# Kernel optimization log

Hardware: AMD Instinct MI355X
Metric: run time of the kernel (lower is better)

## Reference

```python
import jax, jax.numpy as jnp
import numpy as np

HID = 200
HALF = 100  # TreeLSTM hidden = hidden_size // 2
N_EDUS = 32768
N_STEPS = 2 * N_EDUS - 1


def setup_inputs() -> dict:
    key = jax.random.key(0)
    ks = jax.random.split(key, 16)
    s = 0.05  # keep logits / gates in a sane range
    d = {}
    d["enc_cls"] = jax.random.normal(ks[0], (N_EDUS, 768), jnp.float32)
    d["W_proj"] = jax.random.normal(ks[1], (HID, 768), jnp.float32) * s
    d["b_proj"] = jax.random.normal(ks[2], (HID,), jnp.float32) * s
    d["missing_node"] = jax.random.uniform(ks[3], (HID,), jnp.float32)
    d["W_act"] = jax.random.normal(ks[4], (2, 3 * HID), jnp.float32) * s
    d["b_act"] = jax.random.normal(ks[5], (2,), jnp.float32) * s
    d["W_lab"] = jax.random.normal(ks[6], (19, 3 * HID), jnp.float32) * s
    d["b_lab"] = jax.random.normal(ks[7], (19,), jnp.float32) * s
    d["W_dir"] = jax.random.normal(ks[8], (3, 3 * HID), jnp.float32) * s
    d["b_dir"] = jax.random.normal(ks[9], (3,), jnp.float32) * s
    d["W_tree"] = jax.random.normal(ks[10], (5 * HALF, 2 * HALF), jnp.float32) * s
    d["b_tree"] = jax.random.normal(ks[11], (5 * HALF,), jnp.float32) * s
    d["gold_action"] = jax.random.randint(ks[12], (N_STEPS,), 0, 2, jnp.int32)
    d["gold_label"] = jax.random.randint(ks[13], (N_STEPS,), 0, 19, jnp.int32)
    d["gold_direction"] = jax.random.randint(ks[14], (N_STEPS,), 0, 3, jnp.int32)
    return d


def reference(enc_cls, W_proj, b_proj, missing_node, W_act, b_act,
              W_lab, b_lab, W_dir, b_dir, W_tree, b_tree,
              gold_action, gold_label, gold_direction):
    N = enc_cls.shape[0]
    S = 2 * N - 1
    # BERT CLS -> project (dropout is identity in eval)
    enc = enc_cls @ W_proj.T + b_proj  # [N, 200]

    # deterministic left-branching gold schedule: shift, then (shift, reduce)*
    t = jnp.arange(S)
    is_shift = (t == 0) | (t % 2 == 1)

    def treelstm(e1, e2):
        # embeddings are concat(h, c), each HALF
        h1, c1 = e1[:HALF], e1[HALF:]
        h2, c2 = e2[:HALF], e2[HALF:]
        g = W_tree @ jnp.concatenate([h1, h2]) + b_tree  # [5*HALF]
        i, f1, f2, o, u = jnp.split(g, 5)
        c = jax.nn.sigmoid(i) * jnp.tanh(u) \
            + jax.nn.sigmoid(f1) * c1 + jax.nn.sigmoid(f2) * c2
        h = jax.nn.sigmoid(o) * jnp.tanh(c)
        return jnp.concatenate([h, c])

    def ce(logits, y):
        # CrossEntropyLoss for a single example
        return jax.nn.logsumexp(logits) - logits[y]

    def step(carry, xs):
        s1, s0, ptr = carry
        shift, ga, gl, gd = xs
        b = jnp.where(ptr < N, enc[jnp.minimum(ptr, N - 1)], missing_node)
        feats = jnp.concatenate([s1, s0, b])  # [600]
        loss = (ce(W_act @ feats + b_act, ga)
                + ce(W_lab @ feats + b_lab, gl)
                + ce(W_dir @ feats + b_dir, gd))
        merged = treelstm(s1, s0)
        s0n = jnp.where(shift, b, merged)
        s1n = jnp.where(shift, s0, missing_node)
        ptrn = ptr + shift.astype(ptr.dtype)
        return (s1n, s0n, ptrn), loss

    init = (missing_node, missing_node, jnp.int32(0))
    (_, root, _), losses = jax.lax.scan(
        step, init, (is_shift, gold_action, gold_label, gold_direction))
    return losses.sum()
```

## Files before the change

kernel.cpp:

```cpp
#include <hip/hip_runtime.h>
#include <cstdint>

#define HID 200
#define HALF 100
#define N_EDUS 32768
#define N_STEPS (2*N_EDUS - 1)
#define KMAX 32766
#define PSTRIDE 500

typedef __fp16 h2v __attribute__((ext_vector_type(2)));
typedef _Float16 f16x8 __attribute__((ext_vector_type(8)));
typedef float f32x4 __attribute__((ext_vector_type(4)));

__global__ __launch_bounds__(256) void gemm_bt(const float* __restrict__ A, int lda,
    const float* __restrict__ B, int ldb, const float* __restrict__ bias,
    float* __restrict__ C, int ldc, int M, int N, int K)
{
    __shared__ float As[32][68];
    __shared__ float Bs[32][68];
    const int tid = threadIdx.x;
    const int tx = tid & 15, ty = tid >> 4;
    const int m0 = blockIdx.x * 64, n0 = blockIdx.y * 64;
    float acc[4][4] = {};
    for (int kc = 0; kc < K; kc += 32) {
        const int kk = tid & 31, r0 = tid >> 5;
        #pragma unroll
        for (int p = 0; p < 8; ++p) {
            const int mm = r0 + p * 8;
            const int m = m0 + mm, n = n0 + mm, kg = kc + kk;
            As[kk][mm] = (m < M && kg < K) ? A[(size_t)m * lda + kg] : 0.f;
            Bs[kk][mm] = (n < N && kg < K) ? B[(size_t)n * ldb + kg] : 0.f;
        }
        __syncthreads();
        #pragma unroll
        for (int kk2 = 0; kk2 < 32; ++kk2) {
            const float4 a = *(const float4*)&As[kk2][tx * 4];
            const float4 b = *(const float4*)&Bs[kk2][ty * 4];
            const float av[4] = {a.x, a.y, a.z, a.w};
            const float bv[4] = {b.x, b.y, b.z, b.w};
            #pragma unroll
            for (int r = 0; r < 4; ++r)
                #pragma unroll
                for (int c = 0; c < 4; ++c)
                    acc[r][c] += av[r] * bv[c];
        }
        __syncthreads();
    }
    #pragma unroll
    for (int r = 0; r < 4; ++r) {
        const int m = m0 + tx * 4 + r;
        if (m >= M) continue;
        #pragma unroll
        for (int c = 0; c < 4; ++c) {
            const int n = n0 + ty * 4 + c;
            if (n < N) C[(size_t)m * ldc + n] = acc[r][c] + (bias ? bias[n] : 0.f);
        }
    }
}

__global__ void prep_kernel(const float* __restrict__ W_act, const float* __restrict__ W_lab,
    const float* __restrict__ W_dir, const float* __restrict__ miss,
    float* __restrict__ WAB, float* __restrict__ WBC,
    float* __restrict__ msAB, float* __restrict__ msBC, float* __restrict__ out)
{
    const int tid = threadIdx.x;
    if (tid == 0) out[0] = 0.f;
    for (int i = tid; i < 48 * 200; i += 256) {
        const int r = i / 200, c = i % 200;
        const int rr = r % 24;
        const float* src = (rr < 2) ? (W_act + rr * 600)
                         : (rr < 21) ? (W_lab + (rr - 2) * 600)
                                     : (W_dir + (rr - 21) * 600);
        WAB[i] = src[c + (r < 24 ? 0 : 200)];
        WBC[i] = src[c + (r < 24 ? 200 : 400)];
    }
    __syncthreads();
    if (tid < 48) {
        float sA = 0.f, sB = 0.f;
        for (int c = 0; c < 200; ++c) {
            sA += WAB[tid * 200 + c] * miss[c];
            sB += WBC[tid * 200 + c] * miss[c];
        }
        msAB[tid] = sA;
        msBC[tid] = sB;
    }
}

__global__ __launch_bounds__(256) void pack_wb(const float* __restrict__ W_tree,
                                               uint4* __restrict__ WB)
{
    const int i = blockIdx.x * 256 + threadIdx.x;
    if (i >= 8960) return;
    const int lane = i & 63, f = i >> 6;
    const int kc = f & 3, gw = f >> 2;
    const int g = gw % 5, w = gw / 5;
    const int row = w * 16 + (lane & 15);
    const int kb = kc * 32 + (lane >> 4) * 8;
    unsigned int dws[4];
    #pragma unroll
    for (int dw = 0; dw < 4; ++dw) {
        const int k0 = kb + dw * 2;
        float w0 = 0.f, w1 = 0.f;
        if (row < 100) {
            const float* Wr = W_tree + (size_t)(g * 100 + row) * 200;
            if (k0 < 100)     w0 = Wr[k0];
            if (k0 + 1 < 100) w1 = Wr[k0 + 1];
        }
        h2v h = __builtin_amdgcn_cvt_pkrtz(w0, w1);
        __builtin_memcpy(&dws[dw], &h, 4);
    }
    uint4 v; v.x = dws[0]; v.y = dws[1]; v.z = dws[2]; v.w = dws[3];
    WB[i] = v;
}

__device__ __forceinline__ float sigf(float x) {
    return __builtin_amdgcn_rcpf(1.f + __expf(-x));
}
__device__ __forceinline__ float tanhf_(float x) {
    return 1.f - 2.f * __builtin_amdgcn_rcpf(1.f + __expf(2.f * x));
}

#define BAR() asm volatile("s_waitcnt lgkmcnt(0)\n\ts_barrier" ::: "memory")

#define BODY(U, DOLOAD) \
{ \
    const uint4* hb = (const uint4*)(&hbuf[(U) & 1][0]); \
    f16x8 bb[4]; \
    { \
        uint4 t0 = hb[kgrp];      uint4 t1 = hb[4 + kgrp]; \
        uint4 t2 = hb[8 + kgrp];  uint4 t3 = hb[12 + kgrp]; \
        __builtin_memcpy(&bb[0], &t0, 16); __builtin_memcpy(&bb[1], &t1, 16); \
        __builtin_memcpy(&bb[2], &t2, 16); __builtin_memcpy(&bb[3], &t3, 16); \
    } \
    f32x4 aA[5], aB[5]; \
    _Pragma("unroll") \
    for (int g = 0; g < 5; ++g) \
        aA[g] = __builtin_amdgcn_mfma_f32_16x16x32_f16(bb[0], Wf[g][0], z4, 0, 0, 0); \
    _Pragma("unroll") \
    for (int g = 0; g < 5; ++g) \
        aB[g] = __builtin_amdgcn_mfma_f32_16x16x32_f16(bb[2], Wf[g][2], z4, 0, 0, 0); \
    _Pragma("unroll") \
    for (int g = 0; g < 5; ++g) \
        aA[g] = __builtin_amdgcn_mfma_f32_16x16x32_f16(bb[1], Wf[g][1], aA[g], 0, 0, 0); \
    _Pragma("unroll") \
    for (int g = 0; g < 5; ++g) \
        aB[g] = __builtin_amdgcn_mfma_f32_16x16x32_f16(bb[3], Wf[g][3], aB[g], 0, 0, 0); \
    const float gi  = aA[0][0] + aB[0][0] + pr[U][0]; \
    const float gf1 = aA[1][0] + aB[1][0] + pr[U][1]; \
    const float gf2 = aA[2][0] + aB[2][0] + pr[U][2]; \
    const float go  = aA[3][0] + aB[3][0] + pr[U][3]; \
    const float gu  = aA[4][0] + aB[4][0] + pr[U][4]; \
    const float c2v = pr[U][5]; \
    if (DOLOAD) { \
        pr[U][0] = pP[0];   pr[U][1] = pP[100]; pr[U][2] = pP[200]; \
        pr[U][3] = pP[300]; pr[U][4] = pP[400]; pP += PSTRIDE; \
        pr[U][5] = *pE; pE += HID; \
    } \
    const float cnew = sigf(gi) * tanhf_(gu) + sigf(gf1) * c_sel + sigf(gf2) * c2v; \
    const float hnew = sigf(go) * tanhf_(cnew); \
    c_sel = cnew; \
    if (act) { \
        pM[0] = hnew; pM[100] = cnew; \
        hbuf[((U) & 1) ^ 1][r] = (_Float16)hnew; \
    } \
    pM += HID; \
    BAR(); \
}

__attribute__((amdgpu_flat_work_group_size(448, 448), amdgpu_waves_per_eu(2, 2)))
__global__ void chain_kernel(const float* __restrict__ enc,
    const uint4* __restrict__ WB, const float* __restrict__ P, float* __restrict__ M)
{
    const int T = threadIdx.x;
    const int wave = T >> 6, lane = T & 63;
    const int col = lane & 15, kgrp = lane >> 4;
    const int r = wave * 16 + col;
    const int rc = (r < 100) ? r : 99;
    const bool act = (kgrp == 0) && (r < 100);
    __shared__ __align__(16) _Float16 hbuf[2][128];

    if (T < 200) M[T] = enc[T];
    if (T < 128) {
        hbuf[0][T] = (T < 100) ? (_Float16)enc[T] : (_Float16)0.f;
        hbuf[1][T] = (_Float16)0.f;
    }

    f16x8 Wf[5][4];
    #pragma unroll
    for (int g = 0; g < 5; ++g)
        #pragma unroll
        for (int kc = 0; kc < 4; ++kc) {
            uint4 tt = WB[(((wave * 5 + g) * 4) + kc) * 64 + lane];
            __builtin_memcpy(&Wf[g][kc], &tt, 16);
        }
    f32x4 z4 = {0.f, 0.f, 0.f, 0.f};

    float c_sel = enc[100 + rc];

    float pr[4][6];
    #pragma unroll
    for (int u = 0; u < 4; ++u) {
        #pragma unroll
        for (int g = 0; g < 5; ++g)
            pr[u][g] = P[(size_t)(1 + u) * PSTRIDE + g * 100 + rc];
        pr[u][5] = enc[(size_t)(1 + u) * HID + 100 + rc];
    }
    const float* pP = P + (size_t)5 * PSTRIDE + rc;
    const float* pE = enc + (size_t)5 * HID + 100 + rc;
    float* pM = M + HID + r;
    BAR();

    for (int base = 1; base <= KMAX - 9; base += 4) {
        BODY(0, true);
        BODY(1, true);
        BODY(2, true);
        BODY(3, true);
    }
    BODY(0, true);
    BODY(1, true);
    BODY(2, false);
    BODY(3, false);
    BODY(0, false);
    BODY(1, false);
}

__global__ __launch_bounds__(256) void loss_kernel(const float* __restrict__ TM,
    const float* __restrict__ TE, const float* __restrict__ msAB, const float* __restrict__ msBC,
    const float* __restrict__ b_act, const float* __restrict__ b_lab, const float* __restrict__ b_dir,
    const int* __restrict__ ga, const int* __restrict__ gl, const int* __restrict__ gd,
    float* __restrict__ out)
{
    const int t = blockIdx.x * 256 + threadIdx.x;
    float loss = 0.f;
    if (t < N_STEPS) {
        const float *v1, *v0, *vb;
        if (t == 0)      { v1 = msAB; v0 = msAB + 24; vb = TE + 24; }
        else if (t == 1) { v1 = msAB; v0 = TE;        vb = TE + 48 + 24; }
        else if ((t & 1) == 0) {
            const int k = t >> 1;
            v1 = TM + (size_t)(k - 1) * 48;
            v0 = TE + (size_t)k * 48;
            vb = (k < N_EDUS - 1) ? (TE + (size_t)(k + 1) * 48 + 24) : (msBC + 24);
        } else {
            const int k = t >> 1;
            v1 = msAB;
            v0 = TM + (size_t)k * 48 + 24;
            vb = TE + (size_t)(k + 1) * 48 + 24;
        }
        float l[24];
        #pragma unroll
        for (int j = 0; j < 24; ++j) l[j] = v1[j] + v0[j] + vb[j];
        l[0] += b_act[0]; l[1] += b_act[1];
        #pragma unroll
        for (int j = 0; j < 19; ++j) l[2 + j] += b_lab[j];
        #pragma unroll
        for (int j = 0; j < 3; ++j) l[21 + j] += b_dir[j];
        const int ya = ga[t], yl = gl[t], yd = gd[t];
        {
            const float m = fmaxf(l[0], l[1]);
            const float sum = __expf(l[0] - m) + __expf(l[1] - m);
            loss += m + __logf(sum) - (ya == 0 ? l[0] : l[1]);
        }
        {
            float m = l[2];
            #pragma unroll
            for (int j = 1; j < 19; ++j) m = fmaxf(m, l[2 + j]);
            float sum = 0.f, ly = 0.f;
            #pragma unroll
            for (int j = 0; j < 19; ++j) {
                sum += __expf(l[2 + j] - m);
                if (j == yl) ly = l[2 + j];
            }
            loss += m + __logf(sum) - ly;
        }
        {
            const float m = fmaxf(fmaxf(l[21], l[22]), l[23]);
            const float sum = __expf(l[21] - m) + __expf(l[22] - m) + __expf(l[23] - m);
            const float ly = (yd == 0) ? l[21] : (yd == 1 ? l[22] : l[23]);
            loss += m + __logf(sum) - ly;
        }
    }
    #pragma unroll
    for (int off = 32; off > 0; off >>= 1) loss += __shfl_down(loss, off, 64);
    __shared__ float wsum[4];
    const int lane = threadIdx.x & 63, wv = threadIdx.x >> 6;
    if (lane == 0) wsum[wv] = loss;
    __syncthreads();
    if (threadIdx.x == 0) atomicAdd(out, wsum[0] + wsum[1] + wsum[2] + wsum[3]);
}

extern "C" void kernel_launch(void* const* d_in, const int* in_sizes, int n_in,
                              void* d_out, int out_size, void* d_ws, size_t ws_size,
                              hipStream_t stream) {
    const float* enc_cls = (const float*)d_in[0];
    const float* W_proj  = (const float*)d_in[1];
    const float* b_proj  = (const float*)d_in[2];
    const float* miss    = (const float*)d_in[3];
    const float* W_act   = (const float*)d_in[4];
    const float* b_act   = (const float*)d_in[5];
    const float* W_lab   = (const float*)d_in[6];
    const float* b_lab   = (const float*)d_in[7];
    const float* W_dir   = (const float*)d_in[8];
    const float* b_dir   = (const float*)d_in[9];
    const float* W_tree  = (const float*)d_in[10];
    const float* b_tree  = (const float*)d_in[11];
    const int*   ga      = (const int*)d_in[12];
    const int*   gl      = (const int*)d_in[13];
    const int*   gd      = (const int*)d_in[14];
    float* out = (float*)d_out;

    float* ws   = (float*)d_ws;
    float* enc  = ws;
    float* Mar  = ws + 6553600;
    float* P    = ws + 13107000;
    float* WAB  = ws + 29490500;
    float* WBC  = WAB + 9600;
    float* msAB = WBC + 9600;
    float* msBC = msAB + 48;
    uint4* WB   = (uint4*)(msBC + 48);
    float* TM = P;
    float* TE = P + 1572816;

    gemm_bt<<<dim3(512, 4, 1), 256, 0, stream>>>(enc_cls, 768, W_proj, 768, b_proj,
                                                 enc, 200, N_EDUS, 200, 768);
    gemm_bt<<<dim3(512, 8, 1), 256, 0, stream>>>(enc + 200, 200, W_tree + 100, 200, b_tree,
                                                 P + PSTRIDE, PSTRIDE, KMAX, 500, 100);
    prep_kernel<<<1, 256, 0, stream>>>(W_act, W_lab, W_dir, miss, WAB, WBC, msAB, msBC, out);
    pack_wb<<<35, 256, 0, stream>>>(W_tree, WB);
    chain_kernel<<<1, 448, 0, stream>>>(enc, WB, P, Mar);
    gemm_bt<<<dim3(512, 1, 1), 256, 0, stream>>>(Mar, 200, WAB, 200, nullptr,
                                                 TM, 48, KMAX + 1, 48, 200);
    gemm_bt<<<dim3(512, 1, 1), 256, 0, stream>>>(enc, 200, WBC, 200, nullptr,
                                                 TE, 48, N_EDUS, 48, 200);
    loss_kernel<<<dim3(256, 1, 1), 256, 0, stream>>>(TM, TE, msAB, msBC,
                                                     b_act, b_lab, b_dir, ga, gl, gd, out);
}
```

Baseline: 19.33 ms.

## Interleave gate and h/c layouts for vector loads and single MFMA chain

The precomputed gate buffer P is written in an interleaved layout (four gates contiguous per row), so the serial chain kernel fetches them with one float4 plus one scalar load instead of five strided loads. The merged-node output M stores h and c interleaved as a float2, and the loss-side weight matrix WAB and its missing-node dot product are permuted to match. The MFMA accumulation becomes a single dependent chain over the four k-chunks instead of two partial chains, and the prefetch of next-step values moves ahead of the MFMAs. The aim is to cut per-step memory instructions on the latency-bound serial loop, at the cost of a longer MFMA dependency chain.

```diff
diff --git a/kernel.cpp b/kernel.cpp
--- a/kernel.cpp
+++ b/kernel.cpp
@@ -14,7 +14,7 @@
 
 __global__ __launch_bounds__(256) void gemm_bt(const float* __restrict__ A, int lda,
     const float* __restrict__ B, int ldb, const float* __restrict__ bias,
-    float* __restrict__ C, int ldc, int M, int N, int K)
+    float* __restrict__ C, int ldc, int M, int N, int K, int scat)
 {
     __shared__ float As[32][68];
     __shared__ float Bs[32][68];
@@ -53,7 +53,15 @@
         #pragma unroll
         for (int c = 0; c < 4; ++c) {
             const int n = n0 + ty * 4 + c;
-            if (n < N) C[(size_t)m * ldc + n] = acc[r][c] + (bias ? bias[n] : 0.f);
+            if (n < N) {
+                const float v = acc[r][c] + (bias ? bias[n] : 0.f);
+                int col = n;
+                if (scat) {
+                    const int q = n / 100, rr = n - q * 100;
+                    col = (q < 4) ? rr * 4 + q : 400 + rr;
+                }
+                C[(size_t)m * ldc + col] = v;
+            }
         }
     }
 }
@@ -71,14 +79,15 @@
         const float* src = (rr < 2) ? (W_act + rr * 600)
                          : (rr < 21) ? (W_lab + (rr - 2) * 600)
                                      : (W_dir + (rr - 21) * 600);
-        WAB[i] = src[c + (r < 24 ? 0 : 200)];
+        const int ci = (c >> 1) + (c & 1) * 100;
+        WAB[i] = src[ci + (r < 24 ? 0 : 200)];
         WBC[i] = src[c + (r < 24 ? 200 : 400)];
     }
     __syncthreads();
     if (tid < 48) {
         float sA = 0.f, sB = 0.f;
         for (int c = 0; c < 200; ++c) {
-            sA += WAB[tid * 200 + c] * miss[c];
+            sA += WAB[tid * 200 + c] * miss[(c >> 1) + (c & 1) * 100];
             sB += WBC[tid * 200 + c] * miss[c];
         }
         msAB[tid] = sA;
@@ -132,35 +141,35 @@
         __builtin_memcpy(&bb[0], &t0, 16); __builtin_memcpy(&bb[1], &t1, 16); \
         __builtin_memcpy(&bb[2], &t2, 16); __builtin_memcpy(&bb[3], &t3, 16); \
     } \
-    f32x4 aA[5], aB[5]; \
+    const float p0 = pr[U][0], p1 = pr[U][1], p2 = pr[U][2]; \
+    const float p3 = pr[U][3], p4 = pr[U][4], c2v = pr[U][5]; \
+    if (DOLOAD) { \
+        const float4 g4 = *(const float4*)pP4; \
+        pr[U][0] = g4.x; pr[U][1] = g4.y; pr[U][2] = g4.z; pr[U][3] = g4.w; \
+        pr[U][4] = *pPu; \
+        pP4 += PSTRIDE; pPu += PSTRIDE; \
+        pr[U][5] = *pE; pE += HID; \
+    } \
+    f32x4 acc[5]; \
     _Pragma("unroll") \
     for (int g = 0; g < 5; ++g) \
-        aA[g] = __builtin_amdgcn_mfma_f32_16x16x32_f16(bb[0], Wf[g][0], z4, 0, 0, 0); \
+        acc[g] = __builtin_amdgcn_mfma_f32_16x16x32_f16(bb[0], Wf[g][0], z4, 0, 0, 0); \
     _Pragma("unroll") \
-    for (int g = 0; g < 5; ++g) \
-        aB[g] = __builtin_amdgcn_mfma_f32_16x16x32_f16(bb[2], Wf[g][2], z4, 0, 0, 0); \
-    _Pragma("unroll") \
-    for (int g = 0; g < 5; ++g) \
-        aA[g] = __builtin_amdgcn_mfma_f32_16x16x32_f16(bb[1], Wf[g][1], aA[g], 0, 0, 0); \
-    _Pragma("unroll") \
-    for (int g = 0; g < 5; ++g) \
-        aB[g] = __builtin_amdgcn_mfma_f32_16x16x32_f16(bb[3], Wf[g][3], aB[g], 0, 0, 0); \
-    const float gi  = aA[0][0] + aB[0][0] + pr[U][0]; \
-    const float gf1 = aA[1][0] + aB[1][0] + pr[U][1]; \
-    const float gf2 = aA[2][0] + aB[2][0] + pr[U][2]; \
-    const float go  = aA[3][0] + aB[3][0] + pr[U][3]; \
-    const float gu  = aA[4][0] + aB[4][0] + pr[U][4]; \
-    const float c2v = pr[U][5]; \
-    if (DOLOAD) { \
-        pr[U][0] = pP[0];   pr[U][1] = pP[100]; pr[U][2] = pP[200]; \
-        pr[U][3] = pP[300]; pr[U][4] = pP[400]; pP += PSTRIDE; \
-        pr[U][5] = *pE; pE += HID; \
-    } \
+    for (int kc = 1; kc < 4; ++kc) \
+        _Pragma("unroll") \
+        for (int g = 0; g < 5; ++g) \
+            acc[g] = __builtin_amdgcn_mfma_f32_16x16x32_f16(bb[kc], Wf[g][kc], acc[g], 0, 0, 0); \
+    const float gi  = acc[0][0] + p0; \
+    const float gf1 = acc[1][0] + p1; \
+    const float gf2 = acc[2][0] + p2; \
+    const float go  = acc[3][0] + p3; \
+    const float gu  = acc[4][0] + p4; \
     const float cnew = sigf(gi) * tanhf_(gu) + sigf(gf1) * c_sel + sigf(gf2) * c2v; \
     const float hnew = sigf(go) * tanhf_(cnew); \
     c_sel = cnew; \
     if (act) { \
-        pM[0] = hnew; pM[100] = cnew; \
+        float2 hc; hc.x = hnew; hc.y = cnew; \
+        *(float2*)pM = hc; \
         hbuf[((U) & 1) ^ 1][r] = (_Float16)hnew; \
     } \
     pM += HID; \
@@ -179,7 +188,10 @@
     const bool act = (kgrp == 0) && (r < 100);
     __shared__ __align__(16) _Float16 hbuf[2][128];
 
-    if (T < 200) M[T] = enc[T];
+    if (T < 100) {
+        float2 hc; hc.x = enc[T]; hc.y = enc[100 + T];
+        *(float2*)(M + 2 * T) = hc;
+    }
     if (T < 128) {
         hbuf[0][T] = (T < 100) ? (_Float16)enc[T] : (_Float16)0.f;
         hbuf[1][T] = (_Float16)0.f;
@@ -200,14 +212,16 @@
     float pr[4][6];
     #pragma unroll
     for (int u = 0; u < 4; ++u) {
-        #pragma unroll
-        for (int g = 0; g < 5; ++g)
-            pr[u][g] = P[(size_t)(1 + u) * PSTRIDE + g * 100 + rc];
+        const float* pu4 = P + (size_t)(1 + u) * PSTRIDE + rc * 4;
+        const float4 g4 = *(const float4*)pu4;
+        pr[u][0] = g4.x; pr[u][1] = g4.y; pr[u][2] = g4.z; pr[u][3] = g4.w;
+        pr[u][4] = P[(size_t)(1 + u) * PSTRIDE + 400 + rc];
         pr[u][5] = enc[(size_t)(1 + u) * HID + 100 + rc];
     }
-    const float* pP = P + (size_t)5 * PSTRIDE + rc;
-    const float* pE = enc + (size_t)5 * HID + 100 + rc;
-    float* pM = M + HID + r;
+    const float* pP4 = P + (size_t)5 * PSTRIDE + rc * 4;
+    const float* pPu = P + (size_t)5 * PSTRIDE + 400 + rc;
+    const float* pE  = enc + (size_t)5 * HID + 100 + rc;
+    float* pM = M + HID + 2 * r;
     BAR();
 
     for (int base = 1; base <= KMAX - 9; base += 4) {
@@ -322,16 +336,16 @@
     float* TE = P + 1572816;
 
     gemm_bt<<<dim3(512, 4, 1), 256, 0, stream>>>(enc_cls, 768, W_proj, 768, b_proj,
-                                                 enc, 200, N_EDUS, 200, 768);
+                                                 enc, 200, N_EDUS, 200, 768, 0);
     gemm_bt<<<dim3(512, 8, 1), 256, 0, stream>>>(enc + 200, 200, W_tree + 100, 200, b_tree,
-                                                 P + PSTRIDE, PSTRIDE, KMAX, 500, 100);
+                                                 P + PSTRIDE, PSTRIDE, KMAX, 500, 100, 1);
     prep_kernel<<<1, 256, 0, stream>>>(W_act, W_lab, W_dir, miss, WAB, WBC, msAB, msBC, out);
     pack_wb<<<35, 256, 0, stream>>>(W_tree, WB);
     chain_kernel<<<1, 448, 0, stream>>>(enc, WB, P, Mar);
     gemm_bt<<<dim3(512, 1, 1), 256, 0, stream>>>(Mar, 200, WAB, 200, nullptr,
-                                                 TM, 48, KMAX + 1, 48, 200);
+                                                 TM, 48, KMAX + 1, 48, 200, 0);
     gemm_bt<<<dim3(512, 1, 1), 256, 0, stream>>>(enc, 200, WBC, 200, nullptr,
-                                                 TE, 48, N_EDUS, 48, 200);
+                                                 TE, 48, N_EDUS, 48, 200, 0);
     loss_kernel<<<dim3(256, 1, 1), 256, 0, stream>>>(TM, TE, msAB, msBC,
                                                      b_act, b_lab, b_dir, ga, gl, gd, out);
 }
```

After: 17.10 ms. -11.5%, faster.
